# Optimization experiments

Hardware: AMD Instinct MI355X
Metric: run time of the kernel (lower is better)

The kernel has to match this reference:

```python
import jax, jax.numpy as jnp
import numpy as np

N, M = 100000, 800000
F_IN, F_E, H = 64, 16, 64
T_NODE, T_EDGE = 2, 3
HEAD_DIM = 16.0


def setup_inputs() -> dict:
    key = jax.random.key(0)
    ks = jax.random.split(key, 16)
    inp = {
        "x": jax.random.normal(ks[0], (N, F_IN), jnp.float32),
        "edge_feat": jax.random.normal(ks[1], (M, F_E), jnp.float32),
        "node_type": jax.random.randint(ks[2], (N,), 0, T_NODE, jnp.int32),
        "edge_src": jax.random.randint(ks[3], (M,), 0, N, jnp.int32),
        "edge_dst": jax.random.randint(ks[4], (M,), 0, N, jnp.int32),
        "edge_type": jax.random.randint(ks[5], (M,), 0, T_EDGE, jnp.int32),
    }
    s_n = 1.0 / np.sqrt(F_IN)
    s_e = 1.0 / np.sqrt(F_E)
    for i, name in enumerate(["W1", "W2", "W3", "W4"]):
        inp[name] = jax.random.normal(ks[6 + i], (T_NODE, F_IN, H), jnp.float32) * s_n
        inp["b" + name[1]] = jax.random.normal(ks[10 + i], (T_NODE, H), jnp.float32) * 0.01
    inp["W5"] = jax.random.normal(ks[14], (T_EDGE, F_E, H), jnp.float32) * s_e
    inp["b5"] = jax.random.normal(ks[15], (T_EDGE, H), jnp.float32) * 0.01
    return inp


def _node_proj(x, W, b, node_type):
    # per-node-type linear: [T,F,H] weights, select row per node type
    p = jnp.einsum('nf,tfh->tnh', x, W) + b[:, None, :]      # [T,N,H]
    return jnp.take_along_axis(p, node_type[None, :, None], axis=0)[0]  # [N,H]


def reference(x, edge_feat, W1, b1, W2, b2, W3, b3, W4, b4, W5, b5,
              node_type, edge_src, edge_dst, edge_type):
    n = x.shape[0]
    h1 = _node_proj(x, W1, b1, node_type)
    h2 = _node_proj(x, W2, b2, node_type)
    h3 = _node_proj(x, W3, b3, node_type)
    h4 = _node_proj(x, W4, b4, node_type)
    # per-edge-type linear via weight gather (F_E is small)
    w5e = jnp.einsum('mf,mfh->mh', edge_feat, W5[edge_type]) + b5[edge_type]  # [M,H]
    # scalar attention logit per edge (w3_i . (w4_j + w5_ij)) / sqrt(head_dim)
    num = jnp.sum(h3[edge_dst] * (h4[edge_src] + w5e), axis=-1)  # [M]
    # softmax over a single scalar per edge == 1.0 exactly (faithful to source)
    score = jax.nn.softmax((num / jnp.sqrt(HEAD_DIM))[:, None], axis=-1)[:, 0]  # [M]
    msg = score[:, None] * (h2[edge_src] + w5e)                  # [M,H]
    out = h1 + jax.ops.segment_sum(msg, edge_dst, num_segments=n)
    return out
```

## Files before the change

kernel.cpp:

```cpp
#include <hip/hip_runtime.h>


#define CAP 16
#define OVF_CAP 32768

typedef __attribute__((ext_vector_type(8))) short short8;
typedef __attribute__((ext_vector_type(4))) float f32x4;

__device__ __forceinline__ float b2f(unsigned short u) {
    union { unsigned v; float f; } x; x.v = ((unsigned)u) << 16; return x.f;
}
__device__ __forceinline__ unsigned short f2b(float f) {
    union { float f; unsigned v; } x; x.f = f;
    unsigned u = x.v;
    unsigned r = (u + 0x7FFFu + ((u >> 16) & 1u)) >> 16;
    return (unsigned short)r;
}

__global__ __launch_bounds__(256) void bucket_scatter_kernel(
    const int* __restrict__ node_type,
    const int* __restrict__ esrc, const int* __restrict__ edst,
    const int* __restrict__ etype,
    int* __restrict__ perm, int* __restrict__ cnt,
    int* __restrict__ cnt32, int* __restrict__ ovfCnt,
    int4* __restrict__ ovf, int2* __restrict__ rec,
    int N, int M, int nodeBlocks)
{
    int tid = threadIdx.x;
    if (blockIdx.x < (unsigned)nodeBlocks) {
        int i = blockIdx.x * 256 + tid;
        int lane = tid & 63;
        bool act = i < N;
        int t = act ? node_type[i] : -1;
        unsigned long long m0 = __ballot(act && (t == 0));
        unsigned long long m1 = __ballot(act && (t > 0));
        unsigned long long lt = (lane == 0) ? 0ull : ((~0ull) >> (64 - lane));
        if (act) {
            if (t == 0) {
                int cw = __popcll(m0), pre = __popcll(m0 & lt);
                int ldr = __ffsll(m0) - 1;
                int base = 0;
                if (lane == ldr) base = atomicAdd(&cnt[0], cw);
                base = __shfl(base, ldr);
                perm[base + pre] = i;
            } else {
                int cw = __popcll(m1), pre = __popcll(m1 & lt);
                int ldr = __ffsll(m1) - 1;
                int base = 0;
                if (lane == ldr) base = atomicAdd(&cnt[1], cw);
                base = __shfl(base, ldr);
                perm[N - 1 - (base + pre)] = i;
            }
        }
        return;
    }
    int e = (blockIdx.x - nodeBlocks) * 256 + tid;
    if (e >= M) return;
    int d = edst[e];
    int pos = atomicAdd(&cnt32[d], 1);
    int packed = esrc[e] | (etype[e] << 20);
    if (pos < CAP) {
        rec[d * CAP + pos] = make_int2(packed, e);
    } else {
        int slot = atomicAdd(ovfCnt, 1);
        if (slot < OVF_CAP) ovf[slot] = make_int4(packed, e, d, 0);
    }
}

__global__ __launch_bounds__(256) void node_gemm_kernel(
    const float* __restrict__ x, const int* __restrict__ perm,
    const int* __restrict__ cnt,
    const float* __restrict__ W1, const float* __restrict__ b1,
    const float* __restrict__ W2, const float* __restrict__ b2,
    float* __restrict__ out, unsigned short* __restrict__ h2b,
    int N, int nb)
{
    __shared__ __align__(16) unsigned short sx[128 * 72];
    __shared__ __align__(16) unsigned short sw[2][64 * 72];

    int tid = threadIdx.x;
    int c0 = cnt[0];
    int side = (blockIdx.x >= (unsigned)nb) ? 1 : 0;
    int b = blockIdx.x - side * nb;
    int rowbase = side ? (c0 + b * 128) : (b * 128);
    int rowend  = side ? N : c0;
    if (rowbase >= rowend) return;

    const float* W1t = W1 + side * 4096;
    const float* W2t = W2 + side * 4096;

#pragma unroll
    for (int j = 0; j < 4; ++j) {
        int k  = (tid >> 4) + j * 16;
        int n4 = (tid & 15) * 4;
        float4 w1v = *(const float4*)&W1t[k * 64 + n4];
        float4 w2v = *(const float4*)&W2t[k * 64 + n4];
        sw[0][(n4 + 0) * 72 + k] = f2b(w1v.x);
        sw[0][(n4 + 1) * 72 + k] = f2b(w1v.y);
        sw[0][(n4 + 2) * 72 + k] = f2b(w1v.z);
        sw[0][(n4 + 3) * 72 + k] = f2b(w1v.w);
        sw[1][(n4 + 0) * 72 + k] = f2b(w2v.x);
        sw[1][(n4 + 1) * 72 + k] = f2b(w2v.y);
        sw[1][(n4 + 2) * 72 + k] = f2b(w2v.z);
        sw[1][(n4 + 3) * 72 + k] = f2b(w2v.w);
    }

    int fr = (tid & 15) * 4;
    int ir = tid >> 4;
#pragma unroll
    for (int it = 0; it < 8; ++it) {
        int i = it * 16 + ir;
        int r = rowbase + i;
        float4 v = make_float4(0.f, 0.f, 0.f, 0.f);
        if (r < rowend) {
            int n = perm[r];
            v = *(const float4*)&x[n * 64 + fr];
        }
        ushort4 p;
        p.x = f2b(v.x); p.y = f2b(v.y); p.z = f2b(v.z); p.w = f2b(v.w);
        *(ushort4*)&sx[i * 72 + fr] = p;
    }
    __syncthreads();

    int lane = tid & 63;
    int wid  = tid >> 6;
    int q    = lane >> 4;
    int cc   = lane & 15;
    int m0   = wid * 32;

    f32x4 acc[2][2][4];
#pragma unroll
    for (int mm = 0; mm < 2; ++mm)
#pragma unroll
        for (int s = 0; s < 2; ++s)
#pragma unroll
            for (int t = 0; t < 4; ++t)
                acc[mm][s][t] = (f32x4){0.f, 0.f, 0.f, 0.f};

#pragma unroll
    for (int k0 = 0; k0 < 64; k0 += 32) {
        int ko = k0 + q * 8;
        short8 af[2];
        af[0] = *(short8*)&sx[(m0 + cc) * 72 + ko];
        af[1] = *(short8*)&sx[(m0 + 16 + cc) * 72 + ko];
        short8 bf[2][4];
#pragma unroll
        for (int mm = 0; mm < 2; ++mm)
#pragma unroll
            for (int t = 0; t < 4; ++t)
                bf[mm][t] = *(short8*)&sw[mm][(t * 16 + cc) * 72 + ko];
#pragma unroll
        for (int mm = 0; mm < 2; ++mm)
#pragma unroll
            for (int s = 0; s < 2; ++s)
#pragma unroll
                for (int t = 0; t < 4; ++t)
                    acc[mm][s][t] = __builtin_amdgcn_mfma_f32_16x16x32_bf16(
                        af[s], bf[mm][t], acc[mm][s][t], 0, 0, 0);
    }

    float bia1[4], bia2[4];
#pragma unroll
    for (int t = 0; t < 4; ++t) {
        bia1[t] = b1[side * 64 + t * 16 + cc];
        bia2[t] = b2[side * 64 + t * 16 + cc];
    }

#pragma unroll
    for (int s = 0; s < 2; ++s)
#pragma unroll
        for (int reg = 0; reg < 4; ++reg) {
            int rl = m0 + s * 16 + q * 4 + reg;
            int r = rowbase + rl;
            if (r < rowend) {
                int n = perm[r];
#pragma unroll
                for (int t = 0; t < 4; ++t) {
                    out[n * 64 + t * 16 + cc] = acc[0][s][t][reg] + bia1[t];
                    h2b[n * 64 + t * 16 + cc] = f2b(acc[1][s][t][reg] + bia2[t]);
                }
            }
        }
}

__global__ __launch_bounds__(256) void gather_kernel(
    const float* __restrict__ ef, const int2* __restrict__ rec,
    const int* __restrict__ cnt32,
    const float* __restrict__ W5, const float* __restrict__ b5,
    const unsigned short* __restrict__ h2b, float* __restrict__ out, int N)
{
    __shared__ float sW[3072 + 192];
    __shared__ float sG[4][64];

    int tid = threadIdx.x;
    for (int k = tid; k < 816; k += 256) {
        ((float4*)sW)[k] = (k < 768) ? ((const float4*)W5)[k]
                                     : ((const float4*)b5)[k - 768];
    }
    __syncthreads();

    int lane = tid & 63;
    int wid = __builtin_amdgcn_readfirstlane(tid >> 6);
    int d = blockIdx.x * 4 + wid;
    bool active = d < N;
    int deg = 0;
    if (active) deg = min(cnt32[d], CAP);
    int base = d * CAP;

    int myt = (lane < 48) ? (lane >> 4) : (lane - 48);
    int myf = lane & 15;
    float accH = 0.f, accS = 0.f;

    for (int i = 0; i < deg; i += 8) {
        int nrem = deg - i;
        int2 r[8];
#pragma unroll
        for (int j = 0; j < 8; ++j) {
            int ij = i + j;
            ij = (ij < deg) ? ij : (deg - 1);
            r[j] = rec[base + ij];
        }
        float hv[8], ev[8];
#pragma unroll
        for (int j = 0; j < 8; ++j) {
            int s = r[j].x & 0xFFFFF;
            hv[j] = b2f(h2b[(size_t)s * 64 + lane]);
            ev[j] = ef[(size_t)r[j].y * 16 + myf];
        }
#pragma unroll
        for (int j = 0; j < 8; ++j) {
            int t = (unsigned)r[j].x >> 20;
            bool ok = j < nrem;
            accH += ok ? hv[j] : 0.f;
            float v = (lane < 48) ? ev[j] : 1.0f;
            accS += (ok && (t == myt)) ? v : 0.f;
        }
    }

    sG[wid][lane] = accS;
    float rr = accH;
    const float* g = sG[wid];
#pragma unroll
    for (int j = 0; j < 48; ++j)
        rr = fmaf(g[j], sW[j * 64 + lane], rr);
#pragma unroll
    for (int t = 0; t < 3; ++t)
        rr = fmaf(g[48 + t], sW[3072 + t * 64 + lane], rr);

    if (active)
        out[(size_t)d * 64 + lane] += rr;
}

__global__ __launch_bounds__(256) void fixup_kernel(
    const float* __restrict__ ef, const int4* __restrict__ ovf,
    const int* __restrict__ ovfCnt,
    const float* __restrict__ W5, const float* __restrict__ b5,
    const unsigned short* __restrict__ h2b, float* __restrict__ out)
{
    int novf = min(*ovfCnt, OVF_CAP);
    int lane = threadIdx.x & 63;
    int gw = blockIdx.x * 4 + (threadIdx.x >> 6);
    int nw = gridDim.x * 4;
    for (int r = gw; r < novf; r += nw) {
        int4 o = ovf[r];
        int s = o.x & 0xFFFFF;
        int t = (unsigned)o.x >> 20;
        int e = o.y, d = o.z;
        float acc = b5[t * 64 + lane] + b2f(h2b[(size_t)s * 64 + lane]);
#pragma unroll
        for (int f = 0; f < 16; ++f)
            acc = fmaf(ef[(size_t)e * 16 + f], W5[t * 1024 + f * 64 + lane], acc);
        unsafeAtomicAdd(&out[(size_t)d * 64 + lane], acc);
    }
}

extern "C" void kernel_launch(void* const* d_in, const int* in_sizes, int n_in,
                              void* d_out, int out_size, void* d_ws, size_t ws_size,
                              hipStream_t stream) {
    const float* x  = (const float*)d_in[0];
    const float* ef = (const float*)d_in[1];
    const int* nt   = (const int*)d_in[2];
    const int* es   = (const int*)d_in[3];
    const int* ed   = (const int*)d_in[4];
    const int* et   = (const int*)d_in[5];
    const float* W1 = (const float*)d_in[6];
    const float* b1 = (const float*)d_in[7];
    const float* W2 = (const float*)d_in[8];
    const float* b2 = (const float*)d_in[9];
    const float* W5 = (const float*)d_in[14];
    const float* b5 = (const float*)d_in[15];

    int N = in_sizes[2];
    int M = in_sizes[3];

    char* w = (char*)d_ws;
    size_t off = 0;
    unsigned short* h2b = (unsigned short*)(w + off); off += (size_t)N * 64 * 2;
    off = (off + 255) & ~(size_t)255;
    int2* rec = (int2*)(w + off); off += (size_t)N * CAP * 8;
    int* perm = (int*)(w + off);  off += (size_t)N * 4;
    off = (off + 255) & ~(size_t)255;
    int4* ovf = (int4*)(w + off); off += (size_t)OVF_CAP * 16;
    off = (off + 255) & ~(size_t)255;
    int* cnt    = (int*)(w + off);
    int* ovfCnt = cnt + 2;
    int* cnt32  = (int*)(w + off + 64);
    size_t zeroBytes = 64 + (size_t)N * 4;

    float* out = (float*)d_out;

    hipMemsetAsync(cnt, 0, zeroBytes, stream);

    int nodeBlocks = (N + 255) / 256;
    int edgeBlocks = (M + 255) / 256;
    bucket_scatter_kernel<<<nodeBlocks + edgeBlocks, 256, 0, stream>>>(
        nt, es, ed, et, perm, cnt, cnt32, ovfCnt, ovf, rec, N, M, nodeBlocks);

    int nb = (N + 127) / 128;
    node_gemm_kernel<<<2 * nb, 256, 0, stream>>>(x, perm, cnt, W1, b1, W2, b2,
                                                 out, h2b, N, nb);

    gather_kernel<<<(N + 3) / 4, 256, 0, stream>>>(ef, rec, cnt32,
                                                   W5, b5, h2b, out, N);

    fixup_kernel<<<32, 256, 0, stream>>>(ef, ovf, ovfCnt, W5, b5, h2b, out);
}
```

Baseline: 308.0 us.

## Fuse edge scatter into node GEMM, drop type sort, merge overflow fixup into gather

Removes the node-type permutation sort. Each GEMM block now computes both type-specific projections and selects the right result per row using node_type staged in shared memory. The edge bucketing runs in odd blocks of the same kernel, 4 edges per thread, and the overflow fixup pass becomes extra blocks of the gather kernel, which now uses atomic adds to out. This cuts two launches and the perm indirection on x and out, at the cost of twice the MFMA work and weight-staging LDS in the GEMM, plus atomics on every output row.

```diff
diff --git a/kernel.cpp b/kernel.cpp
--- a/kernel.cpp
+++ b/kernel.cpp
@@ -17,92 +17,90 @@
     return (unsigned short)r;
 }
 
-__global__ __launch_bounds__(256) void bucket_scatter_kernel(
-    const int* __restrict__ node_type,
+__global__ __launch_bounds__(256) void k1_gemm_scatter(
+    const float* __restrict__ x, const int* __restrict__ nt,
+    const float* __restrict__ W1, const float* __restrict__ b1,
+    const float* __restrict__ W2, const float* __restrict__ b2,
     const int* __restrict__ esrc, const int* __restrict__ edst,
     const int* __restrict__ etype,
-    int* __restrict__ perm, int* __restrict__ cnt,
     int* __restrict__ cnt32, int* __restrict__ ovfCnt,
     int4* __restrict__ ovf, int2* __restrict__ rec,
-    int N, int M, int nodeBlocks)
-{
-    int tid = threadIdx.x;
-    if (blockIdx.x < (unsigned)nodeBlocks) {
-        int i = blockIdx.x * 256 + tid;
-        int lane = tid & 63;
-        bool act = i < N;
-        int t = act ? node_type[i] : -1;
-        unsigned long long m0 = __ballot(act && (t == 0));
-        unsigned long long m1 = __ballot(act && (t > 0));
-        unsigned long long lt = (lane == 0) ? 0ull : ((~0ull) >> (64 - lane));
-        if (act) {
-            if (t == 0) {
-                int cw = __popcll(m0), pre = __popcll(m0 & lt);
-                int ldr = __ffsll(m0) - 1;
-                int base = 0;
-                if (lane == ldr) base = atomicAdd(&cnt[0], cw);
-                base = __shfl(base, ldr);
-                perm[base + pre] = i;
-            } else {
-                int cw = __popcll(m1), pre = __popcll(m1 & lt);
-                int ldr = __ffsll(m1) - 1;
-                int base = 0;
-                if (lane == ldr) base = atomicAdd(&cnt[1], cw);
-                base = __shfl(base, ldr);
-                perm[N - 1 - (base + pre)] = i;
-            }
-        }
-        return;
-    }
-    int e = (blockIdx.x - nodeBlocks) * 256 + tid;
-    if (e >= M) return;
-    int d = edst[e];
-    int pos = atomicAdd(&cnt32[d], 1);
-    int packed = esrc[e] | (etype[e] << 20);
-    if (pos < CAP) {
-        rec[d * CAP + pos] = make_int2(packed, e);
-    } else {
-        int slot = atomicAdd(ovfCnt, 1);
-        if (slot < OVF_CAP) ovf[slot] = make_int4(packed, e, d, 0);
-    }
-}
-
-__global__ __launch_bounds__(256) void node_gemm_kernel(
-    const float* __restrict__ x, const int* __restrict__ perm,
-    const int* __restrict__ cnt,
-    const float* __restrict__ W1, const float* __restrict__ b1,
-    const float* __restrict__ W2, const float* __restrict__ b2,
     float* __restrict__ out, unsigned short* __restrict__ h2b,
-    int N, int nb)
+    int N, int M)
 {
     __shared__ __align__(16) unsigned short sx[128 * 72];
-    __shared__ __align__(16) unsigned short sw[2][64 * 72];
+    __shared__ __align__(16) unsigned short sw[4][64 * 72];
+    __shared__ int snt[128];
 
     int tid = threadIdx.x;
-    int c0 = cnt[0];
-    int side = (blockIdx.x >= (unsigned)nb) ? 1 : 0;
-    int b = blockIdx.x - side * nb;
-    int rowbase = side ? (c0 + b * 128) : (b * 128);
-    int rowend  = side ? N : c0;
-    if (rowbase >= rowend) return;
-
-    const float* W1t = W1 + side * 4096;
-    const float* W2t = W2 + side * 4096;
-
+
+    if (blockIdx.x & 1) {
+        int e0 = (blockIdx.x >> 1) * 1024 + tid;
+        int dd[4], ssrc[4], tty[4];
+        bool v[4];
+#pragma unroll
+        for (int j = 0; j < 4; ++j) {
+            int e = e0 + j * 256;
+            v[j] = e < M;
+            int ec = v[j] ? e : 0;
+            dd[j]   = edst[ec];
+            ssrc[j] = esrc[ec];
+            tty[j]  = etype[ec];
+        }
+        int pos[4];
+#pragma unroll
+        for (int j = 0; j < 4; ++j)
+            if (v[j]) pos[j] = atomicAdd(&cnt32[dd[j]], 1);
+#pragma unroll
+        for (int j = 0; j < 4; ++j) {
+            if (!v[j]) continue;
+            int packed = ssrc[j] | (tty[j] << 20);
+            int e = e0 + j * 256;
+            if (pos[j] < CAP) {
+                rec[dd[j] * CAP + pos[j]] = make_int2(packed, e);
+            } else {
+                int slot = atomicAdd(ovfCnt, 1);
+                if (slot < OVF_CAP) ovf[slot] = make_int4(packed, e, dd[j], 0);
+            }
+        }
+        return;
+    }
+
+    int rowbase = (blockIdx.x >> 1) * 128;
+
+    const float* Wm0 = W1;
+    const float* Wm1 = W1 + 4096;
+    const float* Wm2 = W2;
+    const float* Wm3 = W2 + 4096;
 #pragma unroll
     for (int j = 0; j < 4; ++j) {
         int k  = (tid >> 4) + j * 16;
         int n4 = (tid & 15) * 4;
-        float4 w1v = *(const float4*)&W1t[k * 64 + n4];
-        float4 w2v = *(const float4*)&W2t[k * 64 + n4];
-        sw[0][(n4 + 0) * 72 + k] = f2b(w1v.x);
-        sw[0][(n4 + 1) * 72 + k] = f2b(w1v.y);
-        sw[0][(n4 + 2) * 72 + k] = f2b(w1v.z);
-        sw[0][(n4 + 3) * 72 + k] = f2b(w1v.w);
-        sw[1][(n4 + 0) * 72 + k] = f2b(w2v.x);
-        sw[1][(n4 + 1) * 72 + k] = f2b(w2v.y);
-        sw[1][(n4 + 2) * 72 + k] = f2b(w2v.z);
-        sw[1][(n4 + 3) * 72 + k] = f2b(w2v.w);
+        float4 w0 = *(const float4*)&Wm0[k * 64 + n4];
+        float4 w1v = *(const float4*)&Wm1[k * 64 + n4];
+        float4 w2v = *(const float4*)&Wm2[k * 64 + n4];
+        float4 w3 = *(const float4*)&Wm3[k * 64 + n4];
+        sw[0][(n4 + 0) * 72 + k] = f2b(w0.x);
+        sw[0][(n4 + 1) * 72 + k] = f2b(w0.y);
+        sw[0][(n4 + 2) * 72 + k] = f2b(w0.z);
+        sw[0][(n4 + 3) * 72 + k] = f2b(w0.w);
+        sw[1][(n4 + 0) * 72 + k] = f2b(w1v.x);
+        sw[1][(n4 + 1) * 72 + k] = f2b(w1v.y);
+        sw[1][(n4 + 2) * 72 + k] = f2b(w1v.z);
+        sw[1][(n4 + 3) * 72 + k] = f2b(w1v.w);
+        sw[2][(n4 + 0) * 72 + k] = f2b(w2v.x);
+        sw[2][(n4 + 1) * 72 + k] = f2b(w2v.y);
+        sw[2][(n4 + 2) * 72 + k] = f2b(w2v.z);
+        sw[2][(n4 + 3) * 72 + k] = f2b(w2v.w);
+        sw[3][(n4 + 0) * 72 + k] = f2b(w3.x);
+        sw[3][(n4 + 1) * 72 + k] = f2b(w3.y);
+        sw[3][(n4 + 2) * 72 + k] = f2b(w3.z);
+        sw[3][(n4 + 3) * 72 + k] = f2b(w3.w);
+    }
+
+    if (tid < 128) {
+        int r = rowbase + tid;
+        snt[tid] = (r < N) ? nt[r] : 0;
     }
 
     int fr = (tid & 15) * 4;
@@ -112,10 +110,7 @@
         int i = it * 16 + ir;
         int r = rowbase + i;
         float4 v = make_float4(0.f, 0.f, 0.f, 0.f);
-        if (r < rowend) {
-            int n = perm[r];
-            v = *(const float4*)&x[n * 64 + fr];
-        }
+        if (r < N) v = *(const float4*)&x[(size_t)r * 64 + fr];
         ushort4 p;
         p.x = f2b(v.x); p.y = f2b(v.y); p.z = f2b(v.z); p.w = f2b(v.w);
         *(ushort4*)&sx[i * 72 + fr] = p;
@@ -128,9 +123,9 @@
     int cc   = lane & 15;
     int m0   = wid * 32;
 
-    f32x4 acc[2][2][4];
-#pragma unroll
-    for (int mm = 0; mm < 2; ++mm)
+    f32x4 acc[4][2][4];
+#pragma unroll
+    for (int mm = 0; mm < 4; ++mm)
 #pragma unroll
         for (int s = 0; s < 2; ++s)
 #pragma unroll
@@ -140,31 +135,28 @@
 #pragma unroll
     for (int k0 = 0; k0 < 64; k0 += 32) {
         int ko = k0 + q * 8;
-        short8 af[2];
-        af[0] = *(short8*)&sx[(m0 + cc) * 72 + ko];
-        af[1] = *(short8*)&sx[(m0 + 16 + cc) * 72 + ko];
-        short8 bf[2][4];
-#pragma unroll
-        for (int mm = 0; mm < 2; ++mm)
-#pragma unroll
-            for (int t = 0; t < 4; ++t)
-                bf[mm][t] = *(short8*)&sw[mm][(t * 16 + cc) * 72 + ko];
-#pragma unroll
-        for (int mm = 0; mm < 2; ++mm)
-#pragma unroll
-            for (int s = 0; s < 2; ++s)
-#pragma unroll
-                for (int t = 0; t < 4; ++t)
-                    acc[mm][s][t] = __builtin_amdgcn_mfma_f32_16x16x32_bf16(
-                        af[s], bf[mm][t], acc[mm][s][t], 0, 0, 0);
-    }
-
-    float bia1[4], bia2[4];
-#pragma unroll
-    for (int t = 0; t < 4; ++t) {
-        bia1[t] = b1[side * 64 + t * 16 + cc];
-        bia2[t] = b2[side * 64 + t * 16 + cc];
-    }
+        short8 af0 = *(short8*)&sx[(m0 + cc) * 72 + ko];
+        short8 af1 = *(short8*)&sx[(m0 + 16 + cc) * 72 + ko];
+#pragma unroll
+        for (int mm = 0; mm < 4; ++mm)
+#pragma unroll
+            for (int t = 0; t < 4; ++t) {
+                short8 bf = *(short8*)&sw[mm][(t * 16 + cc) * 72 + ko];
+                acc[mm][0][t] = __builtin_amdgcn_mfma_f32_16x16x32_bf16(
+                    af0, bf, acc[mm][0][t], 0, 0, 0);
+                acc[mm][1][t] = __builtin_amdgcn_mfma_f32_16x16x32_bf16(
+                    af1, bf, acc[mm][1][t], 0, 0, 0);
+            }
+    }
+
+    float b1v[2][4], b2v[2][4];
+#pragma unroll
+    for (int ty = 0; ty < 2; ++ty)
+#pragma unroll
+        for (int t = 0; t < 4; ++t) {
+            b1v[ty][t] = b1[ty * 64 + t * 16 + cc];
+            b2v[ty][t] = b2[ty * 64 + t * 16 + cc];
+        }
 
 #pragma unroll
     for (int s = 0; s < 2; ++s)
@@ -172,22 +164,28 @@
         for (int reg = 0; reg < 4; ++reg) {
             int rl = m0 + s * 16 + q * 4 + reg;
             int r = rowbase + rl;
-            if (r < rowend) {
-                int n = perm[r];
+            if (r < N) {
+                int ty = snt[rl];
 #pragma unroll
                 for (int t = 0; t < 4; ++t) {
-                    out[n * 64 + t * 16 + cc] = acc[0][s][t][reg] + bia1[t];
-                    h2b[n * 64 + t * 16 + cc] = f2b(acc[1][s][t][reg] + bia2[t]);
+                    float v1 = (ty ? acc[1][s][t][reg] : acc[0][s][t][reg])
+                               + b1v[ty][t];
+                    float v2 = (ty ? acc[3][s][t][reg] : acc[2][s][t][reg])
+                               + b2v[ty][t];
+                    out[(size_t)r * 64 + t * 16 + cc] = v1;
+                    h2b[(size_t)r * 64 + t * 16 + cc] = f2b(v2);
                 }
             }
         }
 }
 
-__global__ __launch_bounds__(256) void gather_kernel(
+__global__ __launch_bounds__(256) void k2_gather(
     const float* __restrict__ ef, const int2* __restrict__ rec,
     const int* __restrict__ cnt32,
     const float* __restrict__ W5, const float* __restrict__ b5,
-    const unsigned short* __restrict__ h2b, float* __restrict__ out, int N)
+    const int4* __restrict__ ovf, const int* __restrict__ ovfCnt,
+    const unsigned short* __restrict__ h2b, float* __restrict__ out,
+    int N, int gatherBlocks, int ovfBlocks)
 {
     __shared__ float sW[3072 + 192];
     __shared__ float sG[4][64];
@@ -200,7 +198,27 @@
     __syncthreads();
 
     int lane = tid & 63;
-    int wid = __builtin_amdgcn_readfirstlane(tid >> 6);
+    int wid = tid >> 6;
+
+    if (blockIdx.x >= (unsigned)gatherBlocks) {
+        int novf = min(*ovfCnt, OVF_CAP);
+        int gw = (blockIdx.x - gatherBlocks) * 4 + wid;
+        int nw = ovfBlocks * 4;
+        for (int ri = gw; ri < novf; ri += nw) {
+            int4 o = ovf[ri];
+            int s = o.x & 0xFFFFF;
+            int t = (unsigned)o.x >> 20;
+            float acc = sW[3072 + t * 64 + lane] +
+                        b2f(h2b[(size_t)s * 64 + lane]);
+#pragma unroll
+            for (int f = 0; f < 16; ++f)
+                acc = fmaf(ef[(size_t)o.y * 16 + f],
+                           sW[(t * 16 + f) * 64 + lane], acc);
+            unsafeAtomicAdd(&out[(size_t)o.z * 64 + lane], acc);
+        }
+        return;
+    }
+
     int d = blockIdx.x * 4 + wid;
     bool active = d < N;
     int deg = 0;
@@ -248,30 +266,7 @@
         rr = fmaf(g[48 + t], sW[3072 + t * 64 + lane], rr);
 
     if (active)
-        out[(size_t)d * 64 + lane] += rr;
-}
-
-__global__ __launch_bounds__(256) void fixup_kernel(
-    const float* __restrict__ ef, const int4* __restrict__ ovf,
-    const int* __restrict__ ovfCnt,
-    const float* __restrict__ W5, const float* __restrict__ b5,
-    const unsigned short* __restrict__ h2b, float* __restrict__ out)
-{
-    int novf = min(*ovfCnt, OVF_CAP);
-    int lane = threadIdx.x & 63;
-    int gw = blockIdx.x * 4 + (threadIdx.x >> 6);
-    int nw = gridDim.x * 4;
-    for (int r = gw; r < novf; r += nw) {
-        int4 o = ovf[r];
-        int s = o.x & 0xFFFFF;
-        int t = (unsigned)o.x >> 20;
-        int e = o.y, d = o.z;
-        float acc = b5[t * 64 + lane] + b2f(h2b[(size_t)s * 64 + lane]);
-#pragma unroll
-        for (int f = 0; f < 16; ++f)
-            acc = fmaf(ef[(size_t)e * 16 + f], W5[t * 1024 + f * 64 + lane], acc);
-        unsafeAtomicAdd(&out[(size_t)d * 64 + lane], acc);
-    }
+        unsafeAtomicAdd(&out[(size_t)d * 64 + lane], rr);
 }
 
 extern "C" void kernel_launch(void* const* d_in, const int* in_sizes, int n_in,
@@ -298,30 +293,27 @@
     unsigned short* h2b = (unsigned short*)(w + off); off += (size_t)N * 64 * 2;
     off = (off + 255) & ~(size_t)255;
     int2* rec = (int2*)(w + off); off += (size_t)N * CAP * 8;
-    int* perm = (int*)(w + off);  off += (size_t)N * 4;
     off = (off + 255) & ~(size_t)255;
     int4* ovf = (int4*)(w + off); off += (size_t)OVF_CAP * 16;
     off = (off + 255) & ~(size_t)255;
-    int* cnt    = (int*)(w + off);
-    int* ovfCnt = cnt + 2;
+    int* ovfCnt = (int*)(w + off);
     int* cnt32  = (int*)(w + off + 64);
     size_t zeroBytes = 64 + (size_t)N * 4;
 
     float* out = (float*)d_out;
 
-    hipMemsetAsync(cnt, 0, zeroBytes, stream);
-
-    int nodeBlocks = (N + 255) / 256;
-    int edgeBlocks = (M + 255) / 256;
-    bucket_scatter_kernel<<<nodeBlocks + edgeBlocks, 256, 0, stream>>>(
-        nt, es, ed, et, perm, cnt, cnt32, ovfCnt, ovf, rec, N, M, nodeBlocks);
-
-    int nb = (N + 127) / 128;
-    node_gemm_kernel<<<2 * nb, 256, 0, stream>>>(x, perm, cnt, W1, b1, W2, b2,
-                                                 out, h2b, N, nb);
-
-    gather_kernel<<<(N + 3) / 4, 256, 0, stream>>>(ef, rec, cnt32,
-                                                   W5, b5, h2b, out, N);
-
-    fixup_kernel<<<32, 256, 0, stream>>>(ef, ovf, ovfCnt, W5, b5, h2b, out);
-}
+    hipMemsetAsync(ovfCnt, 0, zeroBytes, stream);
+
+    int gemmBlocks    = (N + 127) / 128;
+    int scatterBlocks = (M + 1023) / 1024;
+    int gb1 = 2 * max(gemmBlocks, scatterBlocks);
+    k1_gemm_scatter<<<gb1, 256, 0, stream>>>(
+        x, nt, W1, b1, W2, b2, es, ed, et,
+        cnt32, ovfCnt, ovf, rec, out, h2b, N, M);
+
+    int gatherBlocks = (N + 3) / 4;
+    int ovfBlocks = 32;
+    k2_gather<<<gatherBlocks + ovfBlocks, 256, 0, stream>>>(
+        ef, rec, cnt32, W5, b5, ovf, ovfCnt, h2b, out,
+        N, gatherBlocks, ovfBlocks);
+}
```

Result: no change. 306.6 us (-0.4%).
